# Performance work log

Hardware: AMD Instinct MI355X
Metric: run time of the kernel (lower is better)

The kernel has to match this reference:

```python
import jax, jax.numpy as jnp
import numpy as np

EMBED = 768
HEADS = 12
HEAD_DIM = EMBED // HEADS
HIDDEN = 3072
PATCH = 16
IMG = 224
GRID = IMG // PATCH  # 14
NP = GRID * GRID     # 196 patches per image
N_IMAGES = 4
N_BLOCKS = N_IMAGES - 1
B = 8


def layernorm(x, g, b, eps=1e-5):
    mu = jnp.mean(x, axis=-1, keepdims=True)
    var = jnp.mean(jnp.square(x - mu), axis=-1, keepdims=True)
    return (x - mu) * jax.lax.rsqrt(var + eps) * g + b


def patch_embed(img, w, bias):
    # conv2d(k=patch, stride=patch) == unfold to patches + linear
    Bn = img.shape[0]
    x = img.reshape(Bn, 3, GRID, PATCH, GRID, PATCH)
    x = x.transpose(0, 2, 4, 1, 3, 5).reshape(Bn, NP, 3 * PATCH * PATCH)
    return x @ w.reshape(EMBED, -1).T + bias  # [B, NP, EMBED]


def setup_inputs() -> dict:
    key = jax.random.key(0)
    ks = iter(jax.random.split(key, 64))
    d = {}
    for i in range(N_IMAGES):
        d[f"img{i}"] = jax.random.normal(next(ks), (B, 3, IMG, IMG), jnp.float32)
    d["pe_w"] = jax.random.normal(next(ks), (N_IMAGES, EMBED, 3, PATCH, PATCH)) * 0.02
    d["pe_b"] = jnp.zeros((N_IMAGES, EMBED))
    d["spatial_pos"] = jax.random.normal(next(ks), (1, NP, EMBED // 2))
    d["image_pos"] = jax.random.normal(next(ks), (1, N_IMAGES, EMBED // 2))
    d["ln_attn_g"] = jnp.ones((N_BLOCKS, EMBED)); d["ln_attn_b"] = jnp.zeros((N_BLOCKS, EMBED))
    d["qkv_w"] = jax.random.normal(next(ks), (N_BLOCKS, 3 * EMBED, EMBED)) * 0.02
    d["qkv_b"] = jnp.zeros((N_BLOCKS, 3 * EMBED))
    d["proj_w"] = jax.random.normal(next(ks), (N_BLOCKS, EMBED, EMBED)) * 0.02
    d["proj_b"] = jnp.zeros((N_BLOCKS, EMBED))
    d["ln1_g"] = jnp.ones((N_BLOCKS, EMBED)); d["ln1_b"] = jnp.zeros((N_BLOCKS, EMBED))
    d["fc1_w"] = jax.random.normal(next(ks), (N_BLOCKS, HIDDEN, EMBED)) * 0.02
    d["fc1_b"] = jnp.zeros((N_BLOCKS, HIDDEN))
    d["fc2_w"] = jax.random.normal(next(ks), (N_BLOCKS, EMBED, HIDDEN)) * 0.02
    d["fc2_b"] = jnp.zeros((N_BLOCKS, EMBED))
    d["ln2_g"] = jnp.ones((N_BLOCKS, EMBED)); d["ln2_b"] = jnp.zeros((N_BLOCKS, EMBED))
    d["final_g"] = jnp.ones((EMBED,)); d["final_b"] = jnp.zeros((EMBED,))
    d["head_w1"] = jax.random.normal(next(ks), (EMBED, EMBED)) * 0.02
    d["head_b1"] = jnp.zeros((EMBED,))
    d["head_w2"] = jax.random.normal(next(ks), (PATCH * PATCH, EMBED)) * 0.02
    d["head_b2"] = jnp.zeros((PATCH * PATCH,))
    return d


def _pos_encode(x, spatial_pos, image_pos, img_idx):
    n = x.shape[1]
    sp = spatial_pos[:, :n, :]                       # [1, n, E/2]
    ip = jnp.broadcast_to(image_pos[:, img_idx:img_idx + 1, :], (1, n, EMBED // 2))
    return x + jnp.concatenate([sp, ip], axis=-1)


def _block(x, i, p):
    # pre-norm + manual MHA
    residual = x
    h = layernorm(x, p["ln_attn_g"][i], p["ln_attn_b"][i])
    Bn, N, C = h.shape
    qkv = (h @ p["qkv_w"][i].T + p["qkv_b"][i]).reshape(Bn, N, 3, HEADS, HEAD_DIM)
    q, k, v = (qkv[:, :, j].transpose(0, 2, 1, 3) for j in range(3))  # [B,H,N,d]
    attn = jax.nn.softmax(jnp.einsum("bhnd,bhmd->bhnm", q, k) * HEAD_DIM ** -0.5, axis=-1)
    o = jnp.einsum("bhnm,bhmd->bhnd", attn, v).transpose(0, 2, 1, 3).reshape(Bn, N, C)
    x = residual + (o @ p["proj_w"][i].T + p["proj_b"][i])
    # conv block (1x1 convs == linear over channel dim)
    r = x
    h = layernorm(x, p["ln1_g"][i], p["ln1_b"][i])
    h = jax.nn.gelu(h @ p["fc1_w"][i].T + p["fc1_b"][i], approximate=False)
    h = h @ p["fc2_w"][i].T + p["fc2_b"][i]
    return layernorm(r + h, p["ln2_g"][i], p["ln2_b"][i])


def reference(img0, img1, img2, img3, pe_w, pe_b, spatial_pos, image_pos,
              ln_attn_g, ln_attn_b, qkv_w, qkv_b, proj_w, proj_b,
              ln1_g, ln1_b, fc1_w, fc1_b, fc2_w, fc2_b, ln2_g, ln2_b,
              final_g, final_b, head_w1, head_b1, head_w2, head_b2):
    p = dict(ln_attn_g=ln_attn_g, ln_attn_b=ln_attn_b, qkv_w=qkv_w, qkv_b=qkv_b,
             proj_w=proj_w, proj_b=proj_b, ln1_g=ln1_g, ln1_b=ln1_b,
             fc1_w=fc1_w, fc1_b=fc1_b, fc2_w=fc2_w, fc2_b=fc2_b,
             ln2_g=ln2_g, ln2_b=ln2_b)
    images = [img0, img1, img2, img3]
    x1 = _pos_encode(patch_embed(images[0], pe_w[0], pe_b[0]), spatial_pos, image_pos, 0)
    x2 = _pos_encode(patch_embed(images[1], pe_w[1], pe_b[1]), spatial_pos, image_pos, 1)
    x = jnp.concatenate([x1, x2], axis=1)
    x = _block(x, 0, p)
    for i in range(2, N_IMAGES):
        xn = _pos_encode(patch_embed(images[i], pe_w[i], pe_b[i]), spatial_pos, image_pos, i)
        x = jnp.concatenate([x, xn], axis=1)
        x = _block(x, i - 1, p)
    x = layernorm(x, final_g, final_b)
    x = jnp.mean(x, axis=1)                                  # [B, E]
    h = jax.nn.gelu(x @ head_w1.T + head_b1, approximate=False)
    patches = h @ head_w2.T + head_b2                        # [B, PATCH*PATCH]
    Bn = patches.shape[0]
    pimg = patches.reshape(Bn, 1, PATCH, PATCH, 1, 1)
    pimg = jnp.broadcast_to(pimg, (Bn, 1, PATCH, PATCH, GRID, GRID))
    out = pimg.transpose(0, 1, 4, 2, 5, 3).reshape(Bn, 1, IMG, IMG)
    return out
```

## Files before the change

### kernel.cpp

```cpp
#include <hip/hip_runtime.h>
#include <hip/hip_bf16.h>
#include <math.h>

#define EMBED 768
#define QKVD 2304
#define HEADS 12
#define HD 64
#define HIDDEN 3072
#define NPATCH 196
#define SEQMAX 784
#define NB 8
#define IMGSZ 224
#define GRID 14
#define PATCH 16
#define PSTR 72
#define VROW 832

typedef __hip_bfloat16 bf16;
typedef __attribute__((ext_vector_type(8))) short short8;
typedef __attribute__((ext_vector_type(4))) float f32x4;

__device__ __forceinline__ float b2f(bf16 v) { return __bfloat162float(v); }
__device__ __forceinline__ float geluf(float x) {
    return 0.5f * x * (1.0f + erff(x * 0.70710678118654752f));
}

__device__ __forceinline__ void async16(const bf16* g, bf16* l) {
    __builtin_amdgcn_global_load_lds(
        (const __attribute__((address_space(1))) unsigned int*)g,
        (__attribute__((address_space(3))) unsigned int*)l,
        16, 0, 0);
}

#define WAIT_VM0   0x0F70
#define WAIT_VM3   0x0F73
#define WAIT_VM4   0x0F74
#define WAIT_VM5   0x0F75
#define WAIT_VM6   0x0F76
#define WAIT_LGKM0 0xC07F

__global__ __launch_bounds__(256)
void detect_kernel(const unsigned short* __restrict__ raw, int* __restrict__ flag)
{
    __shared__ int bad;
    if (threadIdx.x == 0) bad = 0;
    __syncthreads();
    for (int i = threadIdx.x; i < 8192; i += 256) {
        unsigned int u = (unsigned int)raw[i] << 16;
        float v = __uint_as_float(u);
        if (!(fabsf(v) <= 1e4f)) bad = 1;
    }
    __syncthreads();
    if (threadIdx.x == 0) *flag = bad;
}

struct CvtF32 {
    const void* src[19];
    int n[19];
    int dstOff[19];
    int blkOff[20];
};
__global__ __launch_bounds__(256)
void convert_f32_all(CvtF32 c, float* __restrict__ base, const int* __restrict__ flag)
{
    int f = *flag;
    int b = blockIdx.x;
    int i = 0;
    #pragma unroll
    for (int j = 0; j < 19; ++j) if (b >= c.blkOff[j + 1]) i = j + 1;
    int e = ((b - c.blkOff[i]) * 256 + threadIdx.x) * 4;
    if (e >= c.n[i]) return;
    float* dst = base + c.dstOff[i] + e;
    if (f) {
        *(float4*)dst = *(const float4*)((const float*)c.src[i] + e);
    } else {
        const bf16* s = (const bf16*)c.src[i] + e;
        dst[0] = b2f(s[0]); dst[1] = b2f(s[1]); dst[2] = b2f(s[2]); dst[3] = b2f(s[3]);
    }
}

struct CvtB16 {
    const void* src[5];
    int n[5];
    int dstOff[5];
    int blkOff[6];
};
__global__ __launch_bounds__(256)
void convert_b16_all(CvtB16 c, bf16* __restrict__ base, const int* __restrict__ flag)
{
    int f = *flag;
    int b = blockIdx.x;
    int i = 0;
    #pragma unroll
    for (int j = 0; j < 5; ++j) if (b >= c.blkOff[j + 1]) i = j + 1;
    int e = ((b - c.blkOff[i]) * 256 + threadIdx.x) * 4;
    if (e >= c.n[i]) return;
    bf16* dst = base + (size_t)c.dstOff[i] + e;
    if (f) {
        float4 v = *(const float4*)((const float*)c.src[i] + e);
        dst[0] = __float2bfloat16(v.x); dst[1] = __float2bfloat16(v.y);
        dst[2] = __float2bfloat16(v.z); dst[3] = __float2bfloat16(v.w);
    } else {
        *(uint2*)dst = *(const uint2*)((const bf16*)c.src[i] + e);
    }
}

template<int MT>
__global__ __launch_bounds__(256, 4)
void mfma_gemm(const bf16* __restrict__ A, const bf16* __restrict__ W,
               const float* __restrict__ bias, const float* __restrict__ add,
               float* __restrict__ outF, float* __restrict__ outF2,
               bf16* __restrict__ outB,
               bf16* __restrict__ Qb, bf16* __restrict__ Kb, bf16* __restrict__ Vb,
               int M, int N, int K, int kpitch, int Ntok, int rowStride,
               int mode, int magic)
{
    constexpr int MI = MT / 32;
    __shared__ __align__(16) bf16 As[2][MT * 32];
    __shared__ __align__(16) bf16 Bs[3][128 * 32];
    int tid = threadIdx.x;
    int lane = tid & 63;
    int wave = tid >> 6;
    int wm = wave & 1, wn = wave >> 1;

    unsigned nx = gridDim.x, ny = gridDim.y;
    unsigned nwg = nx * ny * gridDim.z;
    unsigned orig = blockIdx.x + nx * (blockIdx.y + ny * blockIdx.z);
    unsigned qq = nwg >> 3, rr = nwg & 7;
    unsigned xcd = orig & 7, idx8 = orig >> 3;
    unsigned wg = (xcd < rr ? xcd * (qq + 1) : rr * (qq + 1) + (xcd - rr) * qq) + idx8;
    int bxg = (int)(wg % nx);
    unsigned tmp = wg / nx;
    int byg = (int)(tmp % ny);
    int bzg = (int)(tmp / ny);

    int m0 = byg * MT, n0 = bxg * 128;
    int k0 = bzg * K;

    int lr = lane >> 2;
    int lc = lane & 3;
    int sc = lc ^ ((lr >> 1) & 3);
    int ar0 = (MT / 4) * wave + lr;
    int ma0 = m0 + ar0; if (ma0 >= M) ma0 = M - 1;
    int bx0 = (int)(((unsigned)ma0 * (unsigned)magic) >> 24);
    const bf16* aSrc0 = A + (size_t)(bx0 * rowStride + (ma0 - bx0 * Ntok)) * kpitch + k0 + sc * 8;
    const bf16* aSrc1 = nullptr;
    if constexpr (MT == 128) {
        int ma1 = m0 + ar0 + 16; if (ma1 >= M) ma1 = M - 1;
        int bx1 = (int)(((unsigned)ma1 * (unsigned)magic) >> 24);
        aSrc1 = A + (size_t)(bx1 * rowStride + (ma1 - bx1 * Ntok)) * kpitch + k0 + sc * 8;
    }
    const bf16* bSrc0 = W + (size_t)(n0 + 32 * wave + lr) * kpitch + k0 + sc * 8;
    const bf16* bSrc1 = W + (size_t)(n0 + 32 * wave + 16 + lr) * kpitch + k0 + sc * 8;

    int fr = lane & 15;
    int fq = lane >> 4;
    int sq = fq ^ ((fr >> 1) & 3);
    int aOff = (wm * (MT / 2) + fr) * 32 + sq * 8;
    int bOff = (wn * 64 + fr) * 32 + sq * 8;

    f32x4 acc[MI][4] = {};

    auto stageA = [&](int buf) {
        async16(aSrc0, As[buf] + ((MT / 4) * wave) * 32);
        aSrc0 += 32;
        if constexpr (MT == 128) {
            async16(aSrc1, As[buf] + ((MT / 4) * wave + 16) * 32);
            aSrc1 += 32;
        }
    };
    auto stageB = [&](int buf) {
        async16(bSrc0, Bs[buf] + (32 * wave) * 32);
        async16(bSrc1, Bs[buf] + (32 * wave + 16) * 32);
        bSrc0 += 32; bSrc1 += 32;
    };

    int nIter = K >> 5;
    stageB(0);
    stageA(0);
    stageB(1);

    int cur = 0;
    for (int it = 0; it < nIter; ++it) {
        __builtin_amdgcn_sched_barrier(0);
        __builtin_amdgcn_s_waitcnt(WAIT_LGKM0);
        __builtin_amdgcn_s_barrier();
        if (it + 1 < nIter) stageA((it + 1) & 1);
        if (it + 2 < nIter) {
            int nb = cur + 2; if (nb >= 3) nb -= 3;
            stageB(nb);
            if constexpr (MT == 128) __builtin_amdgcn_s_waitcnt(WAIT_VM6);
            else                     __builtin_amdgcn_s_waitcnt(WAIT_VM5);
        } else if (it + 1 < nIter) {
            if constexpr (MT == 128) __builtin_amdgcn_s_waitcnt(WAIT_VM4);
            else                     __builtin_amdgcn_s_waitcnt(WAIT_VM3);
        } else {
            __builtin_amdgcn_s_waitcnt(WAIT_VM0);
        }
        __builtin_amdgcn_s_barrier();
        __builtin_amdgcn_sched_barrier(0);

        const bf16* aR = As[it & 1] + aOff;
        const bf16* bR = Bs[cur] + bOff;
        short8 af[MI], bfr[4];
        #pragma unroll
        for (int mi = 0; mi < MI; ++mi) af[mi] = *(const short8*)(aR + mi * 16 * 32);
        #pragma unroll
        for (int ni = 0; ni < 4; ++ni) bfr[ni] = *(const short8*)(bR + ni * 16 * 32);
        #pragma unroll
        for (int mi = 0; mi < MI; ++mi)
            #pragma unroll
            for (int ni = 0; ni < 4; ++ni)
                acc[mi][ni] = __builtin_amdgcn_mfma_f32_16x16x32_bf16(
                    af[mi], bfr[ni], acc[mi][ni], 0, 0, 0);
        if (++cur >= 3) cur = 0;
    }

    float* oF = bzg ? outF2 : outF;
    float bsv[4];
    #pragma unroll
    for (int ni = 0; ni < 4; ++ni)
        bsv[ni] = bzg ? 0.f : bias[n0 + wn * 64 + ni * 16 + fr];

    if (mode == 3) {
        bf16* dstb[4]; int hhv[4], dcv[4];
        #pragma unroll
        for (int ni = 0; ni < 4; ++ni) {
            int nb = n0 + wn * 64 + ni * 16;
            int which = (nb >= 1536) ? 2 : (nb >= 768) ? 1 : 0;
            int nnb = nb - which * 768;
            dstb[ni] = (which == 0) ? Qb : (which == 1) ? Kb : Vb;
            hhv[ni] = nnb >> 6;
            dcv[ni] = (nnb & 63) + fr;
        }
        #pragma unroll
        for (int mi = 0; mi < MI; ++mi)
            #pragma unroll
            for (int r = 0; r < 4; ++r) {
                int m = m0 + wm * (MT / 2) + mi * 16 + fq * 4 + r;
                if (m >= M) continue;
                int bx_ = (int)(((unsigned)m * (unsigned)magic) >> 24);
                int t = m - bx_ * Ntok;
                #pragma unroll
                for (int ni = 0; ni < 4; ++ni)
                    dstb[ni][((size_t)(bx_ * HEADS + hhv[ni]) * SEQMAX + t) * HD + dcv[ni]]
                        = __float2bfloat16(acc[mi][ni][r] + bsv[ni]);
            }
    } else {
        #pragma unroll
        for (int mi = 0; mi < MI; ++mi)
            #pragma unroll
            for (int r = 0; r < 4; ++r) {
                int m = m0 + wm * (MT / 2) + mi * 16 + fq * 4 + r;
                if (m >= M) continue;
                int bx_ = (int)(((unsigned)m * (unsigned)magic) >> 24);
                int t = m - bx_ * Ntok;
                size_t rb = (size_t)(bx_ * rowStride + t) * N;
                #pragma unroll
                for (int ni = 0; ni < 4; ++ni) {
                    int n = n0 + wn * 64 + ni * 16 + fr;
                    float v = acc[mi][ni][r] + bsv[ni];
                    if (mode == 0)      oF[rb + n] = v;
                    else if (mode == 1) oF[rb + n] = v + add[rb + n];
                    else                outB[rb + n] = __float2bfloat16(geluf(v));
                }
            }
    }
}

__global__ __launch_bounds__(256)
void gemm_kernel(const float* __restrict__ A, const float* __restrict__ W,
                 const float* __restrict__ bias, const float* __restrict__ add,
                 float* __restrict__ C, int M, int N, int K,
                 int Ntok, int rowStride, int dogelu)
{
    __shared__ __align__(16) float As[16][68];
    __shared__ __align__(16) float Ws[16][68];
    int tid = threadIdx.x;
    int tx = tid & 15, ty = tid >> 4;
    int n0 = blockIdx.x * 64, m0 = blockIdx.y * 64;
    int lrow = tid >> 2;
    int lk   = (tid & 3) << 2;
    int am = m0 + lrow;
    bool aok = (am < M);
    const float* Arow = A;
    if (aok) {
        int pr = (am / Ntok) * rowStride + (am % Ntok);
        Arow = A + (size_t)pr * K;
    }
    int wn = n0 + lrow;
    const float* Wrow = (wn < N) ? (W + (size_t)wn * K) : nullptr;
    float acc[4][4] = {};
    for (int kk = 0; kk < K; kk += 16) {
        float4 av = make_float4(0.f, 0.f, 0.f, 0.f);
        if (aok) av = *(const float4*)(Arow + kk + lk);
        float4 wv = make_float4(0.f, 0.f, 0.f, 0.f);
        if (Wrow) wv = *(const float4*)(Wrow + kk + lk);
        __syncthreads();
        As[lk+0][lrow] = av.x; As[lk+1][lrow] = av.y;
        As[lk+2][lrow] = av.z; As[lk+3][lrow] = av.w;
        Ws[lk+0][lrow] = wv.x; Ws[lk+1][lrow] = wv.y;
        Ws[lk+2][lrow] = wv.z; Ws[lk+3][lrow] = wv.w;
        __syncthreads();
        #pragma unroll
        for (int k = 0; k < 16; ++k) {
            float4 a = *(const float4*)&As[k][ty << 2];
            float4 w = *(const float4*)&Ws[k][tx << 2];
            acc[0][0] += a.x*w.x; acc[0][1] += a.x*w.y; acc[0][2] += a.x*w.z; acc[0][3] += a.x*w.w;
            acc[1][0] += a.y*w.x; acc[1][1] += a.y*w.y; acc[1][2] += a.y*w.z; acc[1][3] += a.y*w.w;
            acc[2][0] += a.z*w.x; acc[2][1] += a.z*w.y; acc[2][2] += a.z*w.z; acc[2][3] += a.z*w.w;
            acc[3][0] += a.w*w.x; acc[3][1] += a.w*w.y; acc[3][2] += a.w*w.z; acc[3][3] += a.w*w.w;
        }
    }
    #pragma unroll
    for (int i = 0; i < 4; ++i) {
        int m = m0 + (ty << 2) + i;
        if (m >= M) continue;
        int pr = (m / Ntok) * rowStride + (m % Ntok);
        float* crow = C + (size_t)pr * N;
        const float* addrow = add ? (add + (size_t)pr * N) : nullptr;
        #pragma unroll
        for (int j = 0; j < 4; ++j) {
            int n = n0 + (tx << 2) + j;
            float v = acc[i][j] + bias[n];
            if (addrow) v += addrow[n];
            if (dogelu) v = geluf(v);
            crow[n] = v;
        }
    }
}

__global__ __launch_bounds__(256)
void ln_bf16_kernel(const float* __restrict__ src, bf16* __restrict__ dst,
                    const float* __restrict__ g, const float* __restrict__ bta, int Ntok)
{
    __shared__ float red[256];
    int blk = blockIdx.x;
    int t = blk % Ntok, b = blk / Ntok;
    size_t row = ((size_t)b * SEQMAX + t) * EMBED;
    int tid = threadIdx.x;
    float v0 = src[row + tid], v1 = src[row + tid + 256], v2 = src[row + tid + 512];
    red[tid] = v0 + v1 + v2;
    __syncthreads();
    for (int off = 128; off; off >>= 1) { if (tid < off) red[tid] += red[tid + off]; __syncthreads(); }
    float mu = red[0] * (1.0f / EMBED);
    __syncthreads();
    float d0 = v0 - mu, d1 = v1 - mu, d2 = v2 - mu;
    red[tid] = d0*d0 + d1*d1 + d2*d2;
    __syncthreads();
    for (int off = 128; off; off >>= 1) { if (tid < off) red[tid] += red[tid + off]; __syncthreads(); }
    float rs = rsqrtf(red[0] * (1.0f / EMBED) + 1e-5f);
    dst[row + tid]       = __float2bfloat16(d0 * rs * g[tid]       + bta[tid]);
    dst[row + tid + 256] = __float2bfloat16(d1 * rs * g[tid + 256] + bta[tid + 256]);
    dst[row + tid + 512] = __float2bfloat16(d2 * rs * g[tid + 512] + bta[tid + 512]);
}

__global__ __launch_bounds__(256)
void ln_kernel(const float* __restrict__ src, float* __restrict__ dst,
               const float* __restrict__ g, const float* __restrict__ bta, int Ntok)
{
    __shared__ float red[256];
    int blk = blockIdx.x;
    int t = blk % Ntok, b = blk / Ntok;
    size_t row = ((size_t)b * SEQMAX + t) * EMBED;
    int tid = threadIdx.x;
    float v0 = src[row + tid], v1 = src[row + tid + 256], v2 = src[row + tid + 512];
    red[tid] = v0 + v1 + v2;
    __syncthreads();
    for (int off = 128; off; off >>= 1) { if (tid < off) red[tid] += red[tid + off]; __syncthreads(); }
    float mu = red[0] * (1.0f / EMBED);
    __syncthreads();
    float d0 = v0 - mu, d1 = v1 - mu, d2 = v2 - mu;
    red[tid] = d0*d0 + d1*d1 + d2*d2;
    __syncthreads();
    for (int off = 128; off; off >>= 1) { if (tid < off) red[tid] += red[tid + off]; __syncthreads(); }
    float rs = rsqrtf(red[0] * (1.0f / EMBED) + 1e-5f);
    dst[row + tid]       = d0 * rs * g[tid]       + bta[tid];
    dst[row + tid + 256] = d1 * rs * g[tid + 256] + bta[tid + 256];
    dst[row + tid + 512] = d2 * rs * g[tid + 512] + bta[tid + 512];
}

__global__ __launch_bounds__(256)
void ln_sum_f32_kernel(const float* __restrict__ pa, const float* __restrict__ pb,
                       float* __restrict__ X, const float* __restrict__ g,
                       const float* __restrict__ bta, int Ntok)
{
    __shared__ float red[256];
    int blk = blockIdx.x;
    int t = blk % Ntok, b = blk / Ntok;
    size_t row = ((size_t)b * SEQMAX + t) * EMBED;
    int tid = threadIdx.x;
    float v0 = pa[row + tid]       + pb[row + tid]       + X[row + tid];
    float v1 = pa[row + tid + 256] + pb[row + tid + 256] + X[row + tid + 256];
    float v2 = pa[row + tid + 512] + pb[row + tid + 512] + X[row + tid + 512];
    red[tid] = v0 + v1 + v2;
    __syncthreads();
    for (int off = 128; off; off >>= 1) { if (tid < off) red[tid] += red[tid + off]; __syncthreads(); }
    float mu = red[0] * (1.0f / EMBED);
    __syncthreads();
    float d0 = v0 - mu, d1 = v1 - mu, d2 = v2 - mu;
    red[tid] = d0*d0 + d1*d1 + d2*d2;
    __syncthreads();
    for (int off = 128; off; off >>= 1) { if (tid < off) red[tid] += red[tid + off]; __syncthreads(); }
    float rs = rsqrtf(red[0] * (1.0f / EMBED) + 1e-5f);
    X[row + tid]       = d0 * rs * g[tid]       + bta[tid];
    X[row + tid + 256] = d1 * rs * g[tid + 256] + bta[tid + 256];
    X[row + tid + 512] = d2 * rs * g[tid + 512] + bta[tid + 512];
}

__global__ __launch_bounds__(256)
void vtrans_kernel(const bf16* __restrict__ Vh, bf16* __restrict__ VT, int Ntok)
{
    __shared__ unsigned short Lt[64 * 66];
    int bh = blockIdx.x;
    int k0 = blockIdx.y * 64;
    const bf16* Vb = Vh + (size_t)bh * SEQMAX * HD;
    int tid = threadIdx.x;
    #pragma unroll
    for (int pass = 0; pass < 8; ++pass) {
        int key_l = (tid >> 5) + pass * 8;
        int d2 = tid & 31;
        unsigned v = 0;
        if (k0 + key_l < Ntok)
            v = *(const unsigned*)(Vb + (size_t)(k0 + key_l) * HD + d2 * 2);
        *(unsigned*)&Lt[key_l * 66 + 2 * d2] = v;
    }
    __syncthreads();
    #pragma unroll
    for (int pass = 0; pass < 8; ++pass) {
        int d = (tid >> 5) + pass * 8;
        int kp = tid & 31;
        unsigned lo = Lt[(2 * kp) * 66 + d];
        unsigned hi = Lt[(2 * kp + 1) * 66 + d];
        *(unsigned*)(VT + ((size_t)bh * HD + d) * VROW + k0 + 2 * kp) = lo | (hi << 16);
    }
}

__global__ __launch_bounds__(256)
void flash_mfma(const bf16* __restrict__ Qh, const bf16* __restrict__ Kh,
                const bf16* __restrict__ VT, bf16* __restrict__ O, int Ntok)
{
    __shared__ __align__(16) unsigned short Plds[4][32 * PSTR];
    int bh = blockIdx.x;
    int b = bh / HEADS, h = bh % HEADS;
    int t0 = blockIdx.y * 128;
    int tid = threadIdx.x;
    int lane = tid & 63, w = tid >> 6;
    int fr = lane & 15, fq = lane >> 4;

    const bf16* Qb = Qh + (size_t)bh * SEQMAX * HD;
    const bf16* Kb = Kh + (size_t)bh * SEQMAX * HD;
    const bf16* Vt = VT + (size_t)bh * HD * VROW;

    short8 aq[2][2];
    #pragma unroll
    for (int qi = 0; qi < 2; ++qi) {
        int tq = t0 + w * 32 + qi * 16 + fr; if (tq >= Ntok) tq = Ntok - 1;
        aq[qi][0] = *(const short8*)(Qb + (size_t)tq * HD + fq * 8);
        aq[qi][1] = *(const short8*)(Qb + (size_t)tq * HD + fq * 8 + 32);
    }

    float lpart[2][4] = {};
    f32x4 oacc[2][4];
    #pragma unroll
    for (int qi = 0; qi < 2; ++qi)
        #pragma unroll
        for (int dg = 0; dg < 4; ++dg) oacc[qi][dg] = (f32x4){0.f, 0.f, 0.f, 0.f};

    unsigned short* Pw = Plds[w];

    for (int k0 = 0; k0 < Ntok; k0 += 64) {
        short8 bk[4][2];
        #pragma unroll
        for (int kg = 0; kg < 4; ++kg) {
            int key = k0 + kg * 16 + fr;
            int keyc = key < Ntok ? key : Ntok - 1;
            bk[kg][0] = *(const short8*)(Kb + (size_t)keyc * HD + fq * 8);
            bk[kg][1] = *(const short8*)(Kb + (size_t)keyc * HD + fq * 8 + 32);
        }
        short8 bv[4][2];
        #pragma unroll
        for (int dg = 0; dg < 4; ++dg) {
            int d = dg * 16 + fr;
            bv[dg][0] = *(const short8*)(Vt + (size_t)d * VROW + k0 + fq * 8);
            bv[dg][1] = *(const short8*)(Vt + (size_t)d * VROW + k0 + fq * 8 + 32);
        }

        float s[2][4][4];
        #pragma unroll
        for (int qi = 0; qi < 2; ++qi)
            #pragma unroll
            for (int kg = 0; kg < 4; ++kg) {
                f32x4 sa = (f32x4){0.f, 0.f, 0.f, 0.f};
                sa = __builtin_amdgcn_mfma_f32_16x16x32_bf16(aq[qi][0], bk[kg][0], sa, 0, 0, 0);
                sa = __builtin_amdgcn_mfma_f32_16x16x32_bf16(aq[qi][1], bk[kg][1], sa, 0, 0, 0);
                #pragma unroll
                for (int r = 0; r < 4; ++r) s[qi][kg][r] = sa[r];
            }

        #pragma unroll
        for (int qi = 0; qi < 2; ++qi)
            #pragma unroll
            for (int kg = 0; kg < 4; ++kg) {
                bool ok = (k0 + kg * 16 + fr) < Ntok;
                #pragma unroll
                for (int r = 0; r < 4; ++r) {
                    float p = ok ? __expf(fminf(s[qi][kg][r] * 0.125f, 80.f)) : 0.f;
                    lpart[qi][r] += p;
                    bf16 pb = __float2bfloat16(p);
                    Pw[(qi * 16 + fq * 4 + r) * PSTR + kg * 16 + fr] = *(unsigned short*)&pb;
                }
            }

        short8 ap[2][2];
        #pragma unroll
        for (int qi = 0; qi < 2; ++qi) {
            ap[qi][0] = *(const short8*)(Pw + (qi * 16 + fr) * PSTR + fq * 8);
            ap[qi][1] = *(const short8*)(Pw + (qi * 16 + fr) * PSTR + fq * 8 + 32);
        }

        #pragma unroll
        for (int qi = 0; qi < 2; ++qi)
            #pragma unroll
            for (int dg = 0; dg < 4; ++dg) {
                oacc[qi][dg] = __builtin_amdgcn_mfma_f32_16x16x32_bf16(
                    ap[qi][0], bv[dg][0], oacc[qi][dg], 0, 0, 0);
                oacc[qi][dg] = __builtin_amdgcn_mfma_f32_16x16x32_bf16(
                    ap[qi][1], bv[dg][1], oacc[qi][dg], 0, 0, 0);
            }
    }

    #pragma unroll
    for (int qi = 0; qi < 2; ++qi)
        #pragma unroll
        for (int r = 0; r < 4; ++r) {
            float l = lpart[qi][r];
            l += __shfl_xor(l, 1); l += __shfl_xor(l, 2);
            l += __shfl_xor(l, 4); l += __shfl_xor(l, 8);
            int t = t0 + w * 32 + qi * 16 + fq * 4 + r;
            if (t >= Ntok) continue;
            float inv = 1.0f / l;
            bf16* dst = O + ((size_t)b * SEQMAX + t) * EMBED + h * HD;
            #pragma unroll
            for (int dg = 0; dg < 4; ++dg)
                dst[dg * 16 + fr] = __float2bfloat16(oacc[qi][dg][r] * inv);
        }
}

__global__ __launch_bounds__(256)
void patch_gather(const void* __restrict__ img, bf16* __restrict__ Ap,
                  const int* __restrict__ flag)
{
    int f = *flag;
    int idx = blockIdx.x * 256 + threadIdx.x;
    if (idx >= NB * NPATCH * EMBED) return;
    int col = idx % EMBED;
    int row = idx / EMBED;
    int t = row % NPATCH, b = row / NPATCH;
    int c = col >> 8;
    int pr = (col >> 4) & 15;
    int pc = col & 15;
    int gr = t / GRID, gc = t % GRID;
    size_t off = ((size_t)(b * 3 + c) * IMGSZ + gr * PATCH + pr) * IMGSZ + gc * PATCH + pc;
    float v = f ? ((const float*)img)[off] : b2f(((const bf16*)img)[off]);
    Ap[idx] = __float2bfloat16(v);
}

__global__ __launch_bounds__(256)
void posadd_kernel(const float* __restrict__ PEO, const float* __restrict__ PEO2,
                   const float* __restrict__ sp, const float* __restrict__ ip,
                   float* __restrict__ X, int imgIdx)
{
    int idx = blockIdx.x * 256 + threadIdx.x;
    if (idx >= NB * NPATCH * EMBED) return;
    int e = idx % EMBED;
    int row = idx / EMBED;
    int t = row % NPATCH, b = row / NPATCH;
    float pos = (e < 384) ? sp[t * 384 + e] : ip[imgIdx * 384 + (e - 384)];
    X[((size_t)b * SEQMAX + imgIdx * NPATCH + t) * EMBED + e] = PEO[idx] + PEO2[idx] + pos;
}

__global__ __launch_bounds__(768)
void mean_kernel(const float* __restrict__ H, float* __restrict__ Mn)
{
    int b = blockIdx.x;
    int e = threadIdx.x;
    float s = 0.f;
    for (int t = 0; t < SEQMAX; ++t) s += H[((size_t)b * SEQMAX + t) * EMBED + e];
    Mn[b * EMBED + e] = s * (1.0f / SEQMAX);
}

__global__ __launch_bounds__(256)
void bcast_kernel(const float* __restrict__ P, void* __restrict__ out,
                  const int* __restrict__ flag)
{
    int f = *flag;
    int idx = blockIdx.x * 256 + threadIdx.x;
    if (idx >= NB * IMGSZ * IMGSZ) return;
    int c = idx % IMGSZ;
    int r = (idx / IMGSZ) % IMGSZ;
    int b = idx / (IMGSZ * IMGSZ);
    float v = P[b * 256 + (r & 15) * 16 + (c & 15)];
    if (f) ((float*)out)[idx] = v;
    else   ((bf16*)out)[idx] = __float2bfloat16(v);
}

extern "C" void kernel_launch(void* const* d_in, const int* in_sizes, int n_in,
                              void* d_out, int out_size, void* d_ws, size_t ws_size,
                              hipStream_t stream)
{
    (void)n_in; (void)out_size; (void)ws_size;
    const void* img[4] = {d_in[0], d_in[1], d_in[2], d_in[3]};

    float* ws = (float*)d_ws;
    int* flag = (int*)ws;

    detect_kernel<<<1, 256, 0, stream>>>((const unsigned short*)d_in[0], flag);

    const bool isBig[28] = {0,0,0,0, 1,0,0,0, 0,0,1,0, 1,0,0,0, 1,0,1,0, 0,0,0,0, 0,0,0,0};
    float* fBase = ws + 16;
    float* fPtr[28] = {};
    CvtF32 cf;
    int fCnt = 0, fBlk = 0;
    cf.blkOff[0] = 0;
    {
        float* p = fBase;
        for (int i = 4; i < 28; ++i) {
            if (isBig[i]) continue;
            fPtr[i] = p;
            int n = in_sizes[i];
            cf.src[fCnt] = d_in[i];
            cf.n[fCnt] = n;
            cf.dstOff[fCnt] = (int)(p - fBase);
            fBlk += (n + 1023) / 1024;
            cf.blkOff[fCnt + 1] = fBlk;
            p += n;
            ++fCnt;
        }
        fBase = ws + 16;
        fPtr[0] = p;
    }
    convert_f32_all<<<fBlk, 256, 0, stream>>>(cf, fBase, flag);

    bf16* bPtr[28] = {};
    bf16* bBase = (bf16*)fPtr[0];
    CvtB16 cb;
    int bCnt = 0, bBlk = 0;
    cb.blkOff[0] = 0;
    float* arenaEnd;
    {
        bf16* p = bBase;
        for (int i = 4; i < 28; ++i) {
            if (!isBig[i]) continue;
            bPtr[i] = p;
            int n = in_sizes[i];
            cb.src[bCnt] = d_in[i];
            cb.n[bCnt] = n;
            cb.dstOff[bCnt] = (int)(p - bBase);
            bBlk += (n + 1023) / 1024;
            cb.blkOff[bCnt + 1] = bBlk;
            p += n;
            ++bCnt;
        }
        size_t off = p - (bf16*)ws;
        off = (off + 7) & ~(size_t)7;
        arenaEnd = (float*)((bf16*)ws + off);
    }
    convert_b16_all<<<bBlk, 256, 0, stream>>>(cb, bBase, flag);

    const bf16* pe_w   = bPtr[4];
    const bf16* qkv_w  = bPtr[10];
    const bf16* proj_w = bPtr[12];
    const bf16* fc1_w  = bPtr[16];
    const bf16* fc2_w  = bPtr[18];
    const float* pe_b      = fPtr[5];
    const float* sp        = fPtr[6];
    const float* ip        = fPtr[7];
    const float* ln_attn_g = fPtr[8];
    const float* ln_attn_b = fPtr[9];
    const float* qkv_b     = fPtr[11];
    const float* proj_b    = fPtr[13];
    const float* ln1_g     = fPtr[14];
    const float* ln1_b     = fPtr[15];
    const float* fc1_b     = fPtr[17];
    const float* fc2_b     = fPtr[19];
    const float* ln2_g     = fPtr[20];
    const float* ln2_b     = fPtr[21];
    const float* final_g   = fPtr[22];
    const float* final_b   = fPtr[23];
    const float* head_w1   = fPtr[24];
    const float* head_b1   = fPtr[25];
    const float* head_w2   = fPtr[26];
    const float* head_b2   = fPtr[27];

    const size_t SEQ = (size_t)NB * SEQMAX * EMBED;
    const size_t HID_ELEMS = (size_t)NB * SEQMAX * HIDDEN;
    const size_t EMB_ELEMS = (size_t)NB * NPATCH * EMBED;
    float* X    = arenaEnd;
    float* H    = X + SEQ;
    float* O    = H + SEQ;
    float* PEO  = O + SEQ;
    float* MEAN = PEO + EMB_ELEMS;
    float* HH   = MEAN + NB * EMBED;
    float* PTCH = HH + NB * EMBED;
    bf16* Hb    = (bf16*)(PTCH + NB * 256 + 16);
    bf16* Ob    = Hb + SEQ;
    bf16* Gb    = Ob + SEQ;
    bf16* PEb   = Gb + HID_ELEMS;
    bf16* Qb    = PEb + EMB_ELEMS;
    bf16* Kb    = Qb + SEQ;
    bf16* Vb    = Kb + SEQ;
    bf16* VTb   = Vb + SEQ;

    const int nEmb = NB * NPATCH * EMBED;

    auto magicOf = [](int d) { return (int)(16777216u / (unsigned)d + 1u); };
    const int mgE = magicOf(NB * NPATCH);

    auto embed = [&](int i) {
        patch_gather<<<(nEmb + 255) / 256, 256, 0, stream>>>(img[i], PEb, flag);
        dim3 g(EMBED / 128, (NB * NPATCH + 63) / 64, 2);
        mfma_gemm<64><<<g, 256, 0, stream>>>(PEb, pe_w + (size_t)i * EMBED * EMBED,
                                             pe_b + i * EMBED, nullptr, PEO, H, nullptr,
                                             nullptr, nullptr, nullptr,
                                             NB * NPATCH, EMBED, EMBED / 2, EMBED,
                                             NB * NPATCH, NB * NPATCH, 0, mgE);
        posadd_kernel<<<(nEmb + 255) / 256, 256, 0, stream>>>(PEO, H, sp, ip, X, i);
    };

    auto block = [&](int i, int Ntok) {
        int M = NB * Ntok;
        int gy64  = (M + 63) / 64;
        int gy128 = (M + 127) / 128;
        int nkt = (Ntok + 63) / 64;
        int nqt = (Ntok + 127) / 128;
        int mg = magicOf(Ntok);
        ln_bf16_kernel<<<M, 256, 0, stream>>>(X, Hb, ln_attn_g + i * EMBED, ln_attn_b + i * EMBED, Ntok);
        mfma_gemm<128><<<dim3(QKVD / 128, gy128), 256, 0, stream>>>(
            Hb, qkv_w + (size_t)i * QKVD * EMBED, qkv_b + i * QKVD, nullptr,
            nullptr, nullptr, nullptr, Qb, Kb, Vb, M, QKVD, EMBED, EMBED,
            Ntok, SEQMAX, 3, mg);
        vtrans_kernel<<<dim3(NB * HEADS, nkt), 256, 0, stream>>>(Vb, VTb, Ntok);
        flash_mfma<<<dim3(NB * HEADS, nqt), 256, 0, stream>>>(Qb, Kb, VTb, Ob, Ntok);
        mfma_gemm<64><<<dim3(EMBED / 128, gy64), 256, 0, stream>>>(
            Ob, proj_w + (size_t)i * EMBED * EMBED, proj_b + i * EMBED, X,
            X, nullptr, nullptr, nullptr, nullptr, nullptr,
            M, EMBED, EMBED, EMBED, Ntok, SEQMAX, 1, mg);
        ln_bf16_kernel<<<M, 256, 0, stream>>>(X, Hb, ln1_g + i * EMBED, ln1_b + i * EMBED, Ntok);
        mfma_gemm<128><<<dim3(HIDDEN / 128, gy128), 256, 0, stream>>>(
            Hb, fc1_w + (size_t)i * HIDDEN * EMBED, fc1_b + i * HIDDEN, nullptr,
            nullptr, nullptr, Gb, nullptr, nullptr, nullptr,
            M, HIDDEN, EMBED, EMBED, Ntok, SEQMAX, 2, mg);
        mfma_gemm<64><<<dim3(EMBED / 128, gy64, 2), 256, 0, stream>>>(
            Gb, fc2_w + (size_t)i * EMBED * HIDDEN, fc2_b + i * EMBED, nullptr,
            O, H, nullptr, nullptr, nullptr, nullptr,
            M, EMBED, HIDDEN / 2, HIDDEN, Ntok, SEQMAX, 0, mg);
        ln_sum_f32_kernel<<<M, 256, 0, stream>>>(O, H, X, ln2_g + i * EMBED, ln2_b + i * EMBED, Ntok);
    };

    embed(0);
    embed(1);
    block(0, 392);
    embed(2);
    block(1, 588);
    embed(3);
    block(2, 784);

    ln_kernel<<<NB * SEQMAX, 256, 0, stream>>>(X, H, final_g, final_b, SEQMAX);
    mean_kernel<<<NB, 768, 0, stream>>>(H, MEAN);
    gemm_kernel<<<dim3(EMBED / 64, 1), 256, 0, stream>>>(
        MEAN, head_w1, head_b1, nullptr, HH, NB, EMBED, EMBED, NB, NB, 1);
    gemm_kernel<<<dim3(256 / 64, 1), 256, 0, stream>>>(
        HH, head_w2, head_b2, nullptr, PTCH, NB, 256, EMBED, NB, NB, 0);
    bcast_kernel<<<(NB * IMGSZ * IMGSZ + 255) / 256, 256, 0, stream>>>(PTCH, d_out, flag);
}
```

Measured before the change: 1.158 ms.

## Split flash attention over key halves and combine partials in separate kernel

The attention kernel now splits the key range into two halves along a new grid z dimension, writing unnormalized fp32 partial outputs and row sums to scratch buffers. A new combine kernel adds the two partials, divides by the summed denominators and writes the bf16 output. This doubles the number of attention workgroups, so more CUs are busy when the query-tile count is small, and K loads are prefetched one tile ahead. The cost is an extra launch, extra fp32 traffic through O/H scratch, and a buffer (Lbuf) placed after VTb that must fit within the arena.

```diff
diff --git a/kernel.cpp b/kernel.cpp
--- a/kernel.cpp
+++ b/kernel.cpp
@@ -438,15 +438,24 @@
 
 __global__ __launch_bounds__(256)
 void flash_mfma(const bf16* __restrict__ Qh, const bf16* __restrict__ Kh,
-                const bf16* __restrict__ VT, bf16* __restrict__ O, int Ntok)
+                const bf16* __restrict__ VT, float* __restrict__ O0,
+                float* __restrict__ O1, float* __restrict__ Lp, int Ntok)
 {
     __shared__ __align__(16) unsigned short Plds[4][32 * PSTR];
     int bh = blockIdx.x;
     int b = bh / HEADS, h = bh % HEADS;
     int t0 = blockIdx.y * 128;
+    int z = blockIdx.z;
     int tid = threadIdx.x;
     int lane = tid & 63, w = tid >> 6;
     int fr = lane & 15, fq = lane >> 4;
+
+    int ntile = (Ntok + 63) >> 6;
+    int half = (ntile + 1) >> 1;
+    int kt0 = z ? half : 0;
+    int kt1 = z ? ntile : half;
+    float* Op = z ? O1 : O0;
+    float* Lz = Lp + (size_t)z * (NB * HEADS * SEQMAX) + (size_t)bh * SEQMAX;
 
     const bf16* Qb = Qh + (size_t)bh * SEQMAX * HD;
     const bf16* Kb = Kh + (size_t)bh * SEQMAX * HD;
@@ -469,15 +478,21 @@
 
     unsigned short* Pw = Plds[w];
 
-    for (int k0 = 0; k0 < Ntok; k0 += 64) {
-        short8 bk[4][2];
+    short8 bk[4][2];
+    auto loadK = [&](int kt) {
+        int kk = kt * 64;
         #pragma unroll
         for (int kg = 0; kg < 4; ++kg) {
-            int key = k0 + kg * 16 + fr;
+            int key = kk + kg * 16 + fr;
             int keyc = key < Ntok ? key : Ntok - 1;
             bk[kg][0] = *(const short8*)(Kb + (size_t)keyc * HD + fq * 8);
             bk[kg][1] = *(const short8*)(Kb + (size_t)keyc * HD + fq * 8 + 32);
         }
+    };
+    loadK(kt0);
+
+    for (int kt = kt0; kt < kt1; ++kt) {
+        int k0 = kt * 64;
         short8 bv[4][2];
         #pragma unroll
         for (int dg = 0; dg < 4; ++dg) {
@@ -497,6 +512,8 @@
                 #pragma unroll
                 for (int r = 0; r < 4; ++r) s[qi][kg][r] = sa[r];
             }
+
+        if (kt + 1 < kt1) loadK(kt + 1);
 
         #pragma unroll
         for (int qi = 0; qi < 2; ++qi)
@@ -539,12 +556,31 @@
             l += __shfl_xor(l, 4); l += __shfl_xor(l, 8);
             int t = t0 + w * 32 + qi * 16 + fq * 4 + r;
             if (t >= Ntok) continue;
-            float inv = 1.0f / l;
-            bf16* dst = O + ((size_t)b * SEQMAX + t) * EMBED + h * HD;
+            float* dst = Op + ((size_t)b * SEQMAX + t) * EMBED + h * HD;
             #pragma unroll
             for (int dg = 0; dg < 4; ++dg)
-                dst[dg * 16 + fr] = __float2bfloat16(oacc[qi][dg][r] * inv);
-        }
+                dst[dg * 16 + fr] = oacc[qi][dg][r];
+            if (fr == 0) Lz[t] = l;
+        }
+}
+
+__global__ __launch_bounds__(256)
+void attn_combine(const float* __restrict__ O0, const float* __restrict__ O1,
+                  const float* __restrict__ Lp, bf16* __restrict__ Ob, int Ntok)
+{
+    int blk = blockIdx.x;
+    int t = blk % Ntok, b = blk / Ntok;
+    size_t row = ((size_t)b * SEQMAX + t) * EMBED;
+    int tid = threadIdx.x;
+    const float* L1 = Lp + NB * HEADS * SEQMAX;
+    #pragma unroll
+    for (int j = 0; j < 3; ++j) {
+        int e = tid + j * 256;
+        int h = e >> 6;
+        size_t li = ((size_t)b * HEADS + h) * SEQMAX + t;
+        float inv = 1.0f / (Lp[li] + L1[li]);
+        Ob[row + e] = __float2bfloat16((O0[row + e] + O1[row + e]) * inv);
+    }
 }
 
 __global__ __launch_bounds__(256)
@@ -711,6 +747,7 @@
     bf16* Kb    = Qb + SEQ;
     bf16* Vb    = Kb + SEQ;
     bf16* VTb   = Vb + SEQ;
+    float* Lbuf = (float*)(VTb + (size_t)NB * HEADS * HD * VROW);
 
     const int nEmb = NB * NPATCH * EMBED;
 
@@ -741,7 +778,9 @@
             nullptr, nullptr, nullptr, Qb, Kb, Vb, M, QKVD, EMBED, EMBED,
             Ntok, SEQMAX, 3, mg);
         vtrans_kernel<<<dim3(NB * HEADS, nkt), 256, 0, stream>>>(Vb, VTb, Ntok);
-        flash_mfma<<<dim3(NB * HEADS, nqt), 256, 0, stream>>>(Qb, Kb, VTb, Ob, Ntok);
+        flash_mfma<<<dim3(NB * HEADS, nqt, 2), 256, 0, stream>>>(
+            Qb, Kb, VTb, O, H, Lbuf, Ntok);
+        attn_combine<<<M, 256, 0, stream>>>(O, H, Lbuf, Ob, Ntok);
         mfma_gemm<64><<<dim3(EMBED / 128, gy64), 256, 0, stream>>>(
             Ob, proj_w + (size_t)i * EMBED * EMBED, proj_b + i * EMBED, X,
             X, nullptr, nullptr, nullptr, nullptr, nullptr,
```

After: 1.182 ms. +2.0%, slower.

## Double-buffer K/V tiles in LDS with async loads and remap blocks for XCD locality

Applied to the files above, without the earlier changes.

The flash attention kernel now stages each 64-key K and V^T tile into XOR-swizzled shared-memory double buffers using async global-to-LDS copies, prefetching the next tile while the current one is computed. This replaces direct per-lane global loads of the MFMA operands. Block indices in both the V transpose and flash kernels are remapped so that blocks sharing a batch/head land on the same XCD (o&7), aiming for better L2 reuse. The cost is extra LDS use, which may lower occupancy, plus two barriers per tile.

```diff
diff --git a/kernel.cpp b/kernel.cpp
--- a/kernel.cpp
+++ b/kernel.cpp
@@ -412,8 +412,10 @@
 void vtrans_kernel(const bf16* __restrict__ Vh, bf16* __restrict__ VT, int Ntok)
 {
     __shared__ unsigned short Lt[64 * 66];
-    int bh = blockIdx.x;
-    int k0 = blockIdx.y * 64;
+    unsigned o = blockIdx.x + gridDim.x * blockIdx.y;
+    unsigned x = o & 7, j = o >> 3;
+    int bh = (int)(x * 12 + j % 12);
+    int k0 = (int)(j / 12) * 64;
     const bf16* Vb = Vh + (size_t)bh * SEQMAX * HD;
     int tid = threadIdx.x;
     #pragma unroll
@@ -440,10 +442,16 @@
 void flash_mfma(const bf16* __restrict__ Qh, const bf16* __restrict__ Kh,
                 const bf16* __restrict__ VT, bf16* __restrict__ O, int Ntok)
 {
+    __shared__ __align__(16) bf16 Ks[2][64 * 64];
+    __shared__ __align__(16) bf16 Vs[2][64 * 64];
     __shared__ __align__(16) unsigned short Plds[4][32 * PSTR];
-    int bh = blockIdx.x;
+
+    unsigned o = blockIdx.x + gridDim.x * blockIdx.y;
+    unsigned x = o & 7, j = o >> 3;
+    int bh = (int)(x * 12 + j % 12);
+    int t0 = (int)(j / 12) * 128;
+
     int b = bh / HEADS, h = bh % HEADS;
-    int t0 = blockIdx.y * 128;
     int tid = threadIdx.x;
     int lane = tid & 63, w = tid >> 6;
     int fr = lane & 15, fq = lane >> 4;
@@ -469,48 +477,61 @@
 
     unsigned short* Pw = Plds[w];
 
-    for (int k0 = 0; k0 < Ntok; k0 += 64) {
-        short8 bk[4][2];
+    int srow = lane >> 3;
+    int sslot = (lane & 7) ^ srow;
+    int ntile = (Ntok + 63) >> 6;
+
+    auto stage = [&](int buf, int kt) {
+        int kk = kt * 64;
+        #pragma unroll
+        for (int c = 0; c < 2; ++c) {
+            int row = 16 * w + c * 8 + srow;
+            int key = kk + row; if (key >= Ntok) key = Ntok - 1;
+            async16(Kb + (size_t)key * HD + sslot * 8, Ks[buf] + (16 * w + c * 8) * 64);
+            async16(Vt + (size_t)row * VROW + kk + sslot * 8, Vs[buf] + (16 * w + c * 8) * 64);
+        }
+    };
+
+    stage(0, 0);
+
+    int rs = fr & 7;
+    for (int kt = 0; kt < ntile; ++kt) {
+        int cur = kt & 1;
+        int k0 = kt * 64;
+        __builtin_amdgcn_sched_barrier(0);
+        __builtin_amdgcn_s_waitcnt(WAIT_LGKM0);
+        __builtin_amdgcn_s_barrier();
+        if (kt + 1 < ntile) {
+            stage(cur ^ 1, kt + 1);
+            __builtin_amdgcn_s_waitcnt(WAIT_VM4);
+        } else {
+            __builtin_amdgcn_s_waitcnt(WAIT_VM0);
+        }
+        __builtin_amdgcn_s_barrier();
+        __builtin_amdgcn_sched_barrier(0);
+
+        const bf16* Kc = Ks[cur];
+        const bf16* Vc = Vs[cur];
+
         #pragma unroll
         for (int kg = 0; kg < 4; ++kg) {
-            int key = k0 + kg * 16 + fr;
-            int keyc = key < Ntok ? key : Ntok - 1;
-            bk[kg][0] = *(const short8*)(Kb + (size_t)keyc * HD + fq * 8);
-            bk[kg][1] = *(const short8*)(Kb + (size_t)keyc * HD + fq * 8 + 32);
-        }
-        short8 bv[4][2];
-        #pragma unroll
-        for (int dg = 0; dg < 4; ++dg) {
-            int d = dg * 16 + fr;
-            bv[dg][0] = *(const short8*)(Vt + (size_t)d * VROW + k0 + fq * 8);
-            bv[dg][1] = *(const short8*)(Vt + (size_t)d * VROW + k0 + fq * 8 + 32);
-        }
-
-        float s[2][4][4];
-        #pragma unroll
-        for (int qi = 0; qi < 2; ++qi)
+            short8 bk0 = *(const short8*)(Kc + (kg * 16 + fr) * 64 + (fq ^ rs) * 8);
+            short8 bk1 = *(const short8*)(Kc + (kg * 16 + fr) * 64 + ((fq + 4) ^ rs) * 8);
+            bool ok = (k0 + kg * 16 + fr) < Ntok;
             #pragma unroll
-            for (int kg = 0; kg < 4; ++kg) {
+            for (int qi = 0; qi < 2; ++qi) {
                 f32x4 sa = (f32x4){0.f, 0.f, 0.f, 0.f};
-                sa = __builtin_amdgcn_mfma_f32_16x16x32_bf16(aq[qi][0], bk[kg][0], sa, 0, 0, 0);
-                sa = __builtin_amdgcn_mfma_f32_16x16x32_bf16(aq[qi][1], bk[kg][1], sa, 0, 0, 0);
-                #pragma unroll
-                for (int r = 0; r < 4; ++r) s[qi][kg][r] = sa[r];
-            }
-
-        #pragma unroll
-        for (int qi = 0; qi < 2; ++qi)
-            #pragma unroll
-            for (int kg = 0; kg < 4; ++kg) {
-                bool ok = (k0 + kg * 16 + fr) < Ntok;
+                sa = __builtin_amdgcn_mfma_f32_16x16x32_bf16(aq[qi][0], bk0, sa, 0, 0, 0);
+                sa = __builtin_amdgcn_mfma_f32_16x16x32_bf16(aq[qi][1], bk1, sa, 0, 0, 0);
                 #pragma unroll
                 for (int r = 0; r < 4; ++r) {
-                    float p = ok ? __expf(fminf(s[qi][kg][r] * 0.125f, 80.f)) : 0.f;
+                    float p = ok ? __expf(fminf(sa[r] * 0.125f, 80.f)) : 0.f;
                     lpart[qi][r] += p;
                     bf16 pb = __float2bfloat16(p);
                     Pw[(qi * 16 + fq * 4 + r) * PSTR + kg * 16 + fr] = *(unsigned short*)&pb;
                 }
             }
+        }
 
         short8 ap[2][2];
         #pragma unroll
@@ -520,14 +541,17 @@
         }
 
         #pragma unroll
-        for (int qi = 0; qi < 2; ++qi)
+        for (int dg = 0; dg < 4; ++dg) {
+            short8 bv0 = *(const short8*)(Vc + (dg * 16 + fr) * 64 + (fq ^ rs) * 8);
+            short8 bv1 = *(const short8*)(Vc + (dg * 16 + fr) * 64 + ((fq + 4) ^ rs) * 8);
             #pragma unroll
-            for (int dg = 0; dg < 4; ++dg) {
+            for (int qi = 0; qi < 2; ++qi) {
                 oacc[qi][dg] = __builtin_amdgcn_mfma_f32_16x16x32_bf16(
-                    ap[qi][0], bv[dg][0], oacc[qi][dg], 0, 0, 0);
+                    ap[qi][0], bv0, oacc[qi][dg], 0, 0, 0);
                 oacc[qi][dg] = __builtin_amdgcn_mfma_f32_16x16x32_bf16(
-                    ap[qi][1], bv[dg][1], oacc[qi][dg], 0, 0, 0);
+                    ap[qi][1], bv1, oacc[qi][dg], 0, 0, 0);
             }
+        }
     }
 
     #pragma unroll
@@ -740,8 +764,8 @@
             Hb, qkv_w + (size_t)i * QKVD * EMBED, qkv_b + i * QKVD, nullptr,
             nullptr, nullptr, nullptr, Qb, Kb, Vb, M, QKVD, EMBED, EMBED,
             Ntok, SEQMAX, 3, mg);
-        vtrans_kernel<<<dim3(NB * HEADS, nkt), 256, 0, stream>>>(Vb, VTb, Ntok);
-        flash_mfma<<<dim3(NB * HEADS, nqt), 256, 0, stream>>>(Qb, Kb, VTb, Ob, Ntok);
+        vtrans_kernel<<<dim3(96, nkt), 256, 0, stream>>>(Vb, VTb, Ntok);
+        flash_mfma<<<dim3(96, nqt), 256, 0, stream>>>(Qb, Kb, VTb, Ob, Ntok);
         mfma_gemm<64><<<dim3(EMBED / 128, gy64), 256, 0, stream>>>(
             Ob, proj_w + (size_t)i * EMBED * EMBED, proj_b + i * EMBED, X,
             X, nullptr, nullptr, nullptr, nullptr, nullptr,
```

New measurement: 1.099 ms. 1.05x faster.
